# Performance work log

Measured on AMD Instinct MI355X. Metric: run time of the kernel, lower is better.

## Reference

```python
import jax, jax.numpy as jnp
import numpy as np

PH, PW = 7, 7
SPATIAL_SCALE = 1.0


def setup_inputs() -> dict:
    key = jax.random.key(0)
    kf, kb, kx, ky = jax.random.split(key, 4)
    B, C, H, W, R = 4, 256, 50, 50, 300
    feature_maps = jax.random.normal(kf, (B, C, H, W), dtype=jnp.float32)
    bidx = jax.random.randint(kb, (R,), 0, B).astype(jnp.float32)
    xs = jax.random.uniform(kx, (R, 2), minval=0.0, maxval=W - 1.0)
    ys = jax.random.uniform(ky, (R, 2), minval=0.0, maxval=H - 1.0)
    x_min = jnp.min(xs, axis=1)
    x_max = jnp.max(xs, axis=1)
    y_min = jnp.min(ys, axis=1)
    y_max = jnp.max(ys, axis=1)
    rois = jnp.stack([x_min, y_min, x_max, y_max, bidx], axis=1)  # [R,5]
    return {"feature_maps": feature_maps, "rois": rois}


def _roi_pool(feature_maps, rois):
    B, C, H, W = feature_maps.shape
    s = SPATIAL_SCALE
    r = rois * s                              # first scale application (as in source)
    batch_idx = r[:, 4].astype(jnp.int32)     # int() truncation of scaled batch index
    # second scale application + round + clamp, faithful to source's double-scaling
    x0 = jnp.clip(jnp.round(r[:, 0] * s), 0, W - 1).astype(jnp.int32)
    x1 = jnp.clip(jnp.round(r[:, 2] * s), 0, W - 1).astype(jnp.int32)
    y0 = jnp.clip(jnp.round(r[:, 1] * s), 0, H - 1).astype(jnp.int32)
    y1 = jnp.clip(jnp.round(r[:, 3] * s), 0, H - 1).astype(jnp.int32)
    x1 = jnp.maximum(x1, x0 + 1)
    y1 = jnp.maximum(y1, y0 + 1)
    roi_w = x1 - x0                           # >= 1, so every adaptive bin is nonempty
    roi_h = y1 - y0

    Kw = -(-W // PW)                          # max adaptive bin width  (ceil(W/PW))
    Kh = -(-H // PH)                          # max adaptive bin height (ceil(H/PH))

    # adaptive_max_pool2d bin edges: start = floor(i*size/out), end = ceil((i+1)*size/out)
    pw = jnp.arange(PW)
    wstart = x0[:, None] + (pw[None, :] * roi_w[:, None]) // PW                       # [R,PW]
    wend = x0[:, None] + ((pw[None, :] + 1) * roi_w[:, None] + PW - 1) // PW          # [R,PW]
    kw = jnp.arange(Kw)
    wpos = wstart[:, :, None] + kw[None, None, :]                                      # [R,PW,Kw]
    widx = jnp.clip(wpos, 0, W - 1)
    wvalid = wpos < wend[:, :, None]

    ph = jnp.arange(PH)
    hstart = y0[:, None] + (ph[None, :] * roi_h[:, None]) // PH
    hend = y0[:, None] + ((ph[None, :] + 1) * roi_h[:, None] + PH - 1) // PH
    kh = jnp.arange(Kh)
    hpos = hstart[:, :, None] + kh[None, None, :]                                      # [R,PH,Kh]
    hidx = jnp.clip(hpos, 0, H - 1)
    hvalid = hpos < hend[:, :, None]

    NEG = jnp.finfo(feature_maps.dtype).min
    fm = feature_maps[batch_idx]              # [R,C,H,W] per-ROI source map

    def gather_w(fm_r, widx_r):               # fm_r [C,H,W], widx_r [PW,Kw]
        return fm_r[:, :, widx_r]             # [C,H,PW,Kw]

    g = jax.vmap(gather_w)(fm, widx)          # [R,C,H,PW,Kw]
    A = jnp.max(jnp.where(wvalid[:, None, None, :, :], g, NEG), axis=-1)  # [R,C,H,PW]

    def gather_h(A_r, hidx_r):                # A_r [C,H,PW], hidx_r [PH,Kh]
        return A_r[:, hidx_r, :]              # [C,PH,Kh,PW]

    g2 = jax.vmap(gather_h)(A, hidx)          # [R,C,PH,Kh,PW]
    out = jnp.max(jnp.where(hvalid[:, None, :, :, None], g2, NEG), axis=3)  # [R,C,PH,PW]
    return out


def reference(feature_maps, rois):
    return _roi_pool(feature_maps, rois)
```

## Files before the change

### kernel.cpp

```cpp
#include <hip/hip_runtime.h>
#include <hip/hip_bf16.h>
#include <float.h>

#define B_  4
#define C_  256
#define H_  50
#define W_  50
#define R_  300
#define PH_ 7
#define PW_ 7
#define S_  (H_ * W_)
#define Q_  (PH_ * PW_)
#define SC_ (S_ * C_)
#define ARRN (B_ * SC_)
#define CE_  32
#define NCE  (C_ / CE_)
#define NWG_POOL (R_ * NCE)

__global__ __launch_bounds__(256) void transpose_tables(
    const float* __restrict__ fm,
    float* __restrict__ fmT,
    float* __restrict__ P2,
    float* __restrict__ P4)
{
    __shared__ float tile[64][69];

    const int b  = blockIdx.z;
    const int c0 = blockIdx.y * 64;
    const int s0 = blockIdx.x * 64;

    const int tx = threadIdx.x;
    const int ty = threadIdx.y;

    if (s0 + tx < S_) {
        #pragma unroll
        for (int j = 0; j < 16; ++j) {
            const int c = c0 + ty + j * 4;
            tile[ty + j * 4][tx] = fm[((size_t)b * C_ + c) * S_ + (s0 + tx)];
        }
    }
    if (tx < 4 && s0 + 64 + tx < S_) {
        #pragma unroll
        for (int j = 0; j < 16; ++j) {
            const int c = c0 + ty + j * 4;
            tile[ty + j * 4][64 + tx] = fm[((size_t)b * C_ + c) * S_ + (s0 + 64 + tx)];
        }
    }
    __syncthreads();

    #pragma unroll
    for (int j = 0; j < 16; ++j) {
        const int s = s0 + ty + j * 4;
        if (s < S_) {
            const int ls  = ty + j * 4;
            const int w   = s % W_;
            const int rem = W_ - 1 - w;
            const float v0 = tile[tx][ls];
            float p2 = (rem >= 1) ? fmaxf(v0, tile[tx][ls + 1]) : v0;
            float p4 = p2;
            if (rem >= 2) p4 = fmaxf(p4, tile[tx][ls + 2]);
            if (rem >= 3) p4 = fmaxf(p4, tile[tx][ls + 3]);

            const size_t o = ((size_t)b * S_ + s) * C_ + (c0 + tx);
            fmT[o] = v0;
            P2[o]  = p2;
            P4[o]  = p4;
        }
    }
}

__device__ __forceinline__ void roi_decode(const float* __restrict__ rois, int r,
                                           int& b, int& x0, int& y0,
                                           int& roi_w, int& roi_h)
{
    const float* rp = rois + r * 5;
    b = (int)rp[4];
    x0      = (int)rintf(rp[0]);
    y0      = (int)rintf(rp[1]);
    int x1  = (int)rintf(rp[2]);
    int y1  = (int)rintf(rp[3]);
    x0 = min(max(x0, 0), W_ - 1);
    x1 = min(max(x1, 0), W_ - 1);
    y0 = min(max(y0, 0), H_ - 1);
    y1 = min(max(y1, 0), H_ - 1);
    x1 = max(x1, x0 + 1);
    y1 = max(y1, y0 + 1);
    roi_w = x1 - x0;
    roi_h = y1 - y0;
}

template<int WH>
__device__ __forceinline__ void pool_bins_e(
    const float* __restrict__ fmT, const float* __restrict__ P2,
    const float* __restrict__ P4, float* __restrict__ buf,
    int wv, int lane, int imgCE,
    int x0, int y0, int roi_w, int roi_h)
{
    const int c    = lane & 31;
    const int half = lane >> 5;

    #pragma unroll 2
    for (int k = 0; k < 25; ++k) {
        const int q = wv + 2 * k;
        if (q < Q_) {
            const int ph = q / PW_;
            const int pw = q - ph * PW_;
            const int ws = x0 + (pw * roi_w) / PW_;
            const int we = x0 + ((pw + 1) * roi_w + PW_ - 1) / PW_;
            const int hs = y0 + (ph * roi_h) / PH_;
            const int he = y0 + ((ph + 1) * roi_h + PH_ - 1) / PH_;
            const int ww = we - ws;

            const int sp = (ww >= 4) ? 4 : ((ww >= 2) ? 2 : 1);
            const float* tb = (ww >= 4) ? P4 : ((ww >= 2) ? P2 : fmT);
            const int col = (half ? (we - sp) : ws) * C_;

            float va[WH];
            #pragma unroll
            for (int kh = 0; kh < WH; ++kh) {
                int row = hs + kh;
                row = (row > he - 1) ? (he - 1) : row;
                va[kh] = tb[imgCE + row * (W_ * C_) + col];
            }
            float m = -FLT_MAX;
            #pragma unroll
            for (int kh = 0; kh < WH; ++kh)
                m = fmaxf(m, va[kh]);

            m = fmaxf(m, __shfl_xor(m, 32));
            if (half == 0)
                buf[q * 33 + c] = m;
        }
    }
}

__global__ __launch_bounds__(128) void roi_pool_tables(
    const float* __restrict__ fmT,
    const float* __restrict__ P2,
    const float* __restrict__ P4,
    const float* __restrict__ rois,
    float* __restrict__ out)
{
    __shared__ float buf[Q_ * 33];

    const int bid = blockIdx.x;
    const int e   = bid & 7;
    const int r   = bid >> 3;

    const int t    = threadIdx.x;
    const int wv   = t >> 6;
    const int lane = t & 63;

    int b, x0, y0, roi_w, roi_h;
    roi_decode(rois, r, b, x0, y0, roi_w, roi_h);

    int whmax = 1;
    #pragma unroll
    for (int i = 0; i < PH_; ++i) {
        const int hs = (i * roi_h) / PH_;
        const int he = ((i + 1) * roi_h + PH_ - 1) / PH_;
        whmax = max(whmax, he - hs);
    }

    const int imgCE = b * SC_ + e * CE_ + (lane & 31);

    switch (whmax) {
        case 1: pool_bins_e<1>(fmT, P2, P4, buf, wv, lane, imgCE, x0, y0, roi_w, roi_h); break;
        case 2: pool_bins_e<2>(fmT, P2, P4, buf, wv, lane, imgCE, x0, y0, roi_w, roi_h); break;
        case 3: pool_bins_e<3>(fmT, P2, P4, buf, wv, lane, imgCE, x0, y0, roi_w, roi_h); break;
        case 4: pool_bins_e<4>(fmT, P2, P4, buf, wv, lane, imgCE, x0, y0, roi_w, roi_h); break;
        case 5: pool_bins_e<5>(fmT, P2, P4, buf, wv, lane, imgCE, x0, y0, roi_w, roi_h); break;
        case 6: pool_bins_e<6>(fmT, P2, P4, buf, wv, lane, imgCE, x0, y0, roi_w, roi_h); break;
        case 7: pool_bins_e<7>(fmT, P2, P4, buf, wv, lane, imgCE, x0, y0, roi_w, roi_h); break;
        default: pool_bins_e<8>(fmT, P2, P4, buf, wv, lane, imgCE, x0, y0, roi_w, roi_h); break;
    }
    __syncthreads();

    float* outp = out + ((size_t)r * C_ + e * CE_) * Q_;
    #pragma unroll
    for (int k = 0; k < 13; ++k) {
        const int idx = k * 128 + t;
        if (idx < CE_ * Q_) {
            const int cl = idx / Q_;
            const int q  = idx - cl * Q_;
            outp[idx] = buf[q * 33 + cl];
        }
    }
}

__global__ __launch_bounds__(256) void roi_pool_naive(
    const float* __restrict__ fm,
    const float* __restrict__ rois,
    float* __restrict__ out)
{
    const int total = R_ * C_ * Q_;
    int t = blockIdx.x * blockDim.x + threadIdx.x;
    if (t >= total) return;
    int q   = t % Q_;
    int tmp = t / Q_;
    int pw  = q % PW_;
    int ph  = q / PW_;
    int c   = tmp % C_;
    int r   = tmp / C_;

    int b, x0, y0, roi_w, roi_h;
    roi_decode(rois, r, b, x0, y0, roi_w, roi_h);

    const int ws = x0 + (pw * roi_w) / PW_;
    const int we = x0 + ((pw + 1) * roi_w + PW_ - 1) / PW_;
    const int hs = y0 + (ph * roi_h) / PH_;
    const int he = y0 + ((ph + 1) * roi_h + PH_ - 1) / PH_;

    const float* p = fm + ((size_t)(b * C_ + c)) * S_;
    float m = -FLT_MAX;
    for (int h = hs; h < he; ++h)
        for (int w = ws; w < we; ++w)
            m = fmaxf(m, p[h * W_ + w]);
    out[t] = m;
}

extern "C" void kernel_launch(void* const* d_in, const int* in_sizes, int n_in,
                              void* d_out, int out_size, void* d_ws, size_t ws_size,
                              hipStream_t stream)
{
    const float* fm   = (const float*)d_in[0];
    const float* rois = (const float*)d_in[1];
    float* out        = (float*)d_out;

    const size_t NEED = 3 * (size_t)ARRN * sizeof(float);

    if (ws_size >= NEED) {
        float* fmT = (float*)d_ws;
        float* P2  = fmT + ARRN;
        float* P4  = P2 + ARRN;
        {
            dim3 grid(40, C_ / 64, B_);
            dim3 block(64, 4, 1);
            transpose_tables<<<grid, block, 0, stream>>>(fm, fmT, P2, P4);
        }
        roi_pool_tables<<<NWG_POOL, 128, 0, stream>>>(fmT, P2, P4, rois, out);
    } else {
        const int total = R_ * C_ * Q_;
        roi_pool_naive<<<(total + 255) / 256, 256, 0, stream>>>(fm, rois, out);
    }
}
```

Baseline: 41.10 us.

## Retile transpose per channel group and use four waves per ROI pool block

The transpose kernel now uses 32-channel by 32-position tiles with a 3-element halo, indexed by channel group, instead of 64x64 tiles. The pool kernel moves from 128 to 256 threads, so four waves each handle a contiguous run of about 12 bins. Tail bins are clamped rather than skipped, so some waves recompute a bin redundantly. Output stores become nontemporal. The aim is more parallelism per ROI block and less cache pollution from output writes, at the cost of more, smaller transpose blocks.

After: 36.49 us. 11.2% less time.

```diff
diff --git a/kernel.cpp b/kernel.cpp
--- a/kernel.cpp
+++ b/kernel.cpp
@@ -14,54 +14,50 @@
 #define SC_ (S_ * C_)
 #define ARRN (B_ * SC_)
 #define CE_  32
-#define NCE  (C_ / CE_)
-#define NWG_POOL (R_ * NCE)
-
-__global__ __launch_bounds__(256) void transpose_tables(
+#define NE_  8
+#define NWG_POOL (R_ * NE_)
+
+__global__ __launch_bounds__(256) void transpose_tables_e(
     const float* __restrict__ fm,
     float* __restrict__ fmT,
     float* __restrict__ P2,
     float* __restrict__ P4)
 {
-    __shared__ float tile[64][69];
-
-    const int b  = blockIdx.z;
-    const int c0 = blockIdx.y * 64;
-    const int s0 = blockIdx.x * 64;
-
-    const int tx = threadIdx.x;
-    const int ty = threadIdx.y;
-
-    if (s0 + tx < S_) {
-        #pragma unroll
-        for (int j = 0; j < 16; ++j) {
-            const int c = c0 + ty + j * 4;
-            tile[ty + j * 4][tx] = fm[((size_t)b * C_ + c) * S_ + (s0 + tx)];
-        }
-    }
-    if (tx < 4 && s0 + 64 + tx < S_) {
-        #pragma unroll
-        for (int j = 0; j < 16; ++j) {
-            const int c = c0 + ty + j * 4;
-            tile[ty + j * 4][64 + tx] = fm[((size_t)b * C_ + c) * S_ + (s0 + 64 + tx)];
-        }
+    __shared__ float tile[CE_][37];
+
+    const int bx = blockIdx.x;
+    const int e  = bx & 7;
+    const int st = bx >> 3;
+    const int b  = blockIdx.y;
+    const int s0 = st * 32;
+    const int t  = threadIdx.x;
+
+    for (int idx = t; idx < CE_ * 35; idx += 256) {
+        const int c  = idx / 35;
+        const int ls = idx - c * 35;
+        const int s  = s0 + ls;
+        if (s < S_)
+            tile[c][ls] = fm[(b * C_ + e * CE_ + c) * S_ + s];
     }
     __syncthreads();
 
+    const int c   = t & 31;
+    const int ls0 = t >> 5;
     #pragma unroll
-    for (int j = 0; j < 16; ++j) {
-        const int s = s0 + ty + j * 4;
+    for (int j = 0; j < 4; ++j) {
+        const int ls = ls0 + j * 8;
+        const int s  = s0 + ls;
         if (s < S_) {
-            const int ls  = ty + j * 4;
-            const int w   = s % W_;
-            const int rem = W_ - 1 - w;
-            const float v0 = tile[tx][ls];
-            float p2 = (rem >= 1) ? fmaxf(v0, tile[tx][ls + 1]) : v0;
+            const int w = s % W_;
+            int rem = W_ - 1 - w;
+            if (rem > 3) rem = 3;
+            const float v0 = tile[c][ls];
+            float p2 = (rem >= 1) ? fmaxf(v0, tile[c][ls + 1]) : v0;
             float p4 = p2;
-            if (rem >= 2) p4 = fmaxf(p4, tile[tx][ls + 2]);
-            if (rem >= 3) p4 = fmaxf(p4, tile[tx][ls + 3]);
-
-            const size_t o = ((size_t)b * S_ + s) * C_ + (c0 + tx);
+            if (rem >= 2) p4 = fmaxf(p4, tile[c][ls + 2]);
+            if (rem >= 3) p4 = fmaxf(p4, tile[c][ls + 3]);
+
+            const int o = (b * S_ + s) * C_ + e * CE_ + c;
             fmT[o] = v0;
             P2[o]  = p2;
             P4[o]  = p4;
@@ -98,43 +94,44 @@
 {
     const int c    = lane & 31;
     const int half = lane >> 5;
+    const int start = wv * 12 + (wv ? 1 : 0);
+    const int qlast = wv * 12 + 12;
 
     #pragma unroll 2
-    for (int k = 0; k < 25; ++k) {
-        const int q = wv + 2 * k;
-        if (q < Q_) {
-            const int ph = q / PW_;
-            const int pw = q - ph * PW_;
-            const int ws = x0 + (pw * roi_w) / PW_;
-            const int we = x0 + ((pw + 1) * roi_w + PW_ - 1) / PW_;
-            const int hs = y0 + (ph * roi_h) / PH_;
-            const int he = y0 + ((ph + 1) * roi_h + PH_ - 1) / PH_;
-            const int ww = we - ws;
-
-            const int sp = (ww >= 4) ? 4 : ((ww >= 2) ? 2 : 1);
-            const float* tb = (ww >= 4) ? P4 : ((ww >= 2) ? P2 : fmT);
-            const int col = (half ? (we - sp) : ws) * C_;
-
-            float va[WH];
-            #pragma unroll
-            for (int kh = 0; kh < WH; ++kh) {
-                int row = hs + kh;
-                row = (row > he - 1) ? (he - 1) : row;
-                va[kh] = tb[imgCE + row * (W_ * C_) + col];
-            }
-            float m = -FLT_MAX;
-            #pragma unroll
-            for (int kh = 0; kh < WH; ++kh)
-                m = fmaxf(m, va[kh]);
-
-            m = fmaxf(m, __shfl_xor(m, 32));
-            if (half == 0)
-                buf[q * 33 + c] = m;
-        }
-    }
-}
-
-__global__ __launch_bounds__(128) void roi_pool_tables(
+    for (int k = 0; k < 13; ++k) {
+        int q = start + k;
+        q = (q > qlast) ? qlast : q;
+        const int ph = q / PW_;
+        const int pw = q - ph * PW_;
+        const int ws = x0 + (pw * roi_w) / PW_;
+        const int we = x0 + ((pw + 1) * roi_w + PW_ - 1) / PW_;
+        const int hs = y0 + (ph * roi_h) / PH_;
+        const int he = y0 + ((ph + 1) * roi_h + PH_ - 1) / PH_;
+        const int ww = we - ws;
+
+        const int sp = (ww >= 4) ? 4 : ((ww >= 2) ? 2 : 1);
+        const float* tb = (ww >= 4) ? P4 : ((ww >= 2) ? P2 : fmT);
+        const int col = (half ? (we - sp) : ws) * C_;
+
+        float va[WH];
+        #pragma unroll
+        for (int kh = 0; kh < WH; ++kh) {
+            int row = hs + kh;
+            row = (row > he - 1) ? (he - 1) : row;
+            va[kh] = tb[imgCE + row * (W_ * C_) + col];
+        }
+        float m = -FLT_MAX;
+        #pragma unroll
+        for (int kh = 0; kh < WH; ++kh)
+            m = fmaxf(m, va[kh]);
+
+        m = fmaxf(m, __shfl_xor(m, 32));
+        if (half == 0)
+            buf[q * 33 + c] = m;
+    }
+}
+
+__global__ __launch_bounds__(256) void roi_pool_e(
     const float* __restrict__ fmT,
     const float* __restrict__ P2,
     const float* __restrict__ P4,
@@ -178,12 +175,12 @@
 
     float* outp = out + ((size_t)r * C_ + e * CE_) * Q_;
     #pragma unroll
-    for (int k = 0; k < 13; ++k) {
-        const int idx = k * 128 + t;
+    for (int k = 0; k < 7; ++k) {
+        const int idx = k * 256 + t;
         if (idx < CE_ * Q_) {
             const int cl = idx / Q_;
             const int q  = idx - cl * Q_;
-            outp[idx] = buf[q * 33 + cl];
+            __builtin_nontemporal_store(buf[q * 33 + cl], &outp[idx]);
         }
     }
 }
@@ -234,11 +231,10 @@
         float* P2  = fmT + ARRN;
         float* P4  = P2 + ARRN;
         {
-            dim3 grid(40, C_ / 64, B_);
-            dim3 block(64, 4, 1);
-            transpose_tables<<<grid, block, 0, stream>>>(fm, fmT, P2, P4);
-        }
-        roi_pool_tables<<<NWG_POOL, 128, 0, stream>>>(fmT, P2, P4, rois, out);
+            dim3 grid(79 * NE_, B_);
+            transpose_tables_e<<<grid, 256, 0, stream>>>(fm, fmT, P2, P4);
+        }
+        roi_pool_e<<<NWG_POOL, 256, 0, stream>>>(fmT, P2, P4, rois, out);
     } else {
         const int total = R_ * C_ * Q_;
         roi_pool_naive<<<(total + 255) / 256, 256, 0, stream>>>(fm, rois, out);
```
